# Performance work log

Measured on AMD Instinct MI355X. Metric: run time of the kernel, lower is better.

The kernel has to match this reference:

```python
import jax, jax.numpy as jnp
import numpy as np

B, N, D_MODEL = 2, 1536, 512
MIN_WL, MAX_WL, BASE = 3.7, 20.0, 20.0
COORD_SCALE = 8.0  # Angstrom-ish spread so pair distances span the wavelength band
EPS = 1e-6


def setup_inputs() -> dict:
    key = jax.random.key(0)
    k1, _ = jax.random.split(key)
    coords = jax.random.normal(k1, (B, N, 3), dtype=jnp.float32) * COORD_SCALE
    key_padding_mask = jnp.zeros((B, N), dtype=bool)  # True = padded
    K = D_MODEL // 2
    # buffer from __init__: min_wl + (max_wl-min_wl)*(logspace(0,1,K,base)-1)/(base-1)
    wavelengths = MIN_WL + (MAX_WL - MIN_WL) * (jnp.logspace(0.0, 1.0, K, base=BASE) - 1.0) / (BASE - 1.0)
    wavenumbers = (2.0 * jnp.pi / wavelengths).astype(jnp.float32)
    return {"coords": coords, "key_padding_mask": key_padding_mask, "wavenumbers": wavenumbers}


def reference(coords, key_padding_mask, wavenumbers):
    # coords: [B,N,3]; key_padding_mask: [B,N] (True = pad); wavenumbers: [K]
    b, n, _ = coords.shape
    diff = coords[:, :, None, :] - coords[:, None, :, :]          # [B,N,N,3]
    r = jnp.sqrt(jnp.sum(diff * diff, axis=-1) + 1e-12)            # [B,N,N]
    # valid sources: not padded and not the point itself (Green's fn singular at r=0)
    valid = (~key_padding_mask)[:, None, :] & (~jnp.eye(n, dtype=bool))[None]
    amp = jnp.where(valid, 1.0 / (4.0 * jnp.pi * jnp.maximum(r, EPS)), 0.0)  # [B,N,N]

    # scan over wavenumbers so we never materialize a [B,N,N,K] tensor
    def step(_, k):
        phase = k * r                                              # [B,N,N]
        re = jnp.sum(jnp.cos(phase) * amp, axis=-1)                # [B,N]
        im = jnp.sum(jnp.sin(phase) * amp, axis=-1)                # [B,N]
        return None, (re, im)

    _, (re, im) = jax.lax.scan(step, None, wavenumbers)            # each [K,B,N]
    wf = jnp.stack([re, im], axis=-1)                              # [K,B,N,2]
    wf = jnp.moveaxis(wf, 0, 2)                                    # [B,N,K,2]
    return wf.reshape(b, n, -1)                                    # [B,N,d_model]
```

## Files before the change

kernel.cpp:

```cpp
#include <hip/hip_runtime.h>
#include <math.h>


#define N_FIXED  1536
#define K_FIXED  256
#define QBINS    256
#define QG       260
#define ROWS     4
#define RSTRIDE  272
#define NTHREADS 512
#define FPSCALE  4194304.0f

typedef __attribute__((ext_vector_type(2))) float f32x2;

__global__ __launch_bounds__(256) void wf_direct_kernel(
    const float* __restrict__ coords, const unsigned char* __restrict__ mask,
    const float* __restrict__ wavenumbers, float* __restrict__ out, int N, int K)
{
    __shared__ float2 pairs[N_FIXED];
    const int row = blockIdx.x;
    const int b   = row / N;
    const int i   = row - b * N;
    const int t   = threadIdx.x;
    const float* crow = coords + (size_t)b * N * 3;
    const float xi = crow[i*3+0], yi = crow[i*3+1], zi = crow[i*3+2];
    const unsigned char* mrow = mask + (size_t)b * N;
    for (int j = t; j < N; j += blockDim.x) {
        float dx = crow[j*3+0]-xi, dy = crow[j*3+1]-yi, dz = crow[j*3+2]-zi;
        float d2 = fmaf(dx,dx, fmaf(dy,dy, fmaf(dz,dz, 1e-12f)));
        float r  = sqrtf(d2);
        float amp = 0.07957747154594767f / fmaxf(r, 1e-6f);
        if (j == i || mrow[j]) amp = 0.0f;
        pairs[j] = make_float2(r, amp);
    }
    __syncthreads();
    const int k = t;
    const float f = wavenumbers[k] * 0.15915494309189535f;
    float re = 0.0f, im = 0.0f;
    #pragma unroll 4
    for (int j = 0; j < N; ++j) {
        float2 p = pairs[j];
        float x  = __builtin_amdgcn_fractf(p.x * f);
        float c  = __builtin_amdgcn_cosf(x);
        float s  = __builtin_amdgcn_sinf(x);
        re = fmaf(c, p.y, re);
        im = fmaf(s, p.y, im);
    }
    float2* orow = (float2*)out + (size_t)row * K;
    orow[k] = make_float2(re, im);
}

__global__ __launch_bounds__(NTHREADS) void wf_fused_kernel(
    const float* __restrict__ coords, const unsigned char* __restrict__ mask,
    const float* __restrict__ wavenumbers, float* __restrict__ out, int N)
{
    __shared__ int   hist[ROWS * RSTRIDE];
    __shared__ float red[8];
    __shared__ f32x2 merge[ROWS * K_FIXED];

    const int i0 = blockIdx.x * ROWS;
    const int b  = i0 / N;
    const int t  = threadIdx.x;

    const float* crow = coords + (size_t)b * N * 3;
    const unsigned char* mrow = mask + (size_t)b * N;

    float m = 0.0f;
    #pragma unroll
    for (int s = 0; s < N_FIXED / NTHREADS; ++s) {
        const int p = t + NTHREADS * s;
        float x = crow[3*p], y = crow[3*p+1], z = crow[3*p+2];
        m = fmaxf(m, fmaf(x,x, fmaf(y,y, z*z)));
    }
    #pragma unroll
    for (int off = 32; off >= 1; off >>= 1)
        m = fmaxf(m, __shfl_down(m, off, 64));
    if ((t & 63) == 0) red[t >> 6] = m;
    for (int a = t; a < ROWS * RSTRIDE; a += NTHREADS) hist[a] = 0;
    __syncthreads();
    float mm = red[0];
    #pragma unroll
    for (int w = 1; w < 8; ++w) mm = fmaxf(mm, red[w]);
    const float rmax = 2.0005f * sqrtf(mm) + 1e-3f;
    const float h    = rmax / (float)QBINS;
    const float inv_h = 1.0f / h;

    const int il0 = i0 - b * N;
    float cx[ROWS], cy[ROWS], cz[ROWS];
    #pragma unroll
    for (int r = 0; r < ROWS; ++r) {
        cx[r] = crow[3*(il0+r)];
        cy[r] = crow[3*(il0+r)+1];
        cz[r] = crow[3*(il0+r)+2];
    }

    #pragma unroll
    for (int s = 0; s < N_FIXED / NTHREADS; ++s) {
        const int j = t + NTHREADS * s;
        const float xj = crow[3*j], yj = crow[3*j+1], zj = crow[3*j+2];
        const bool masked = (mrow[j] != 0);
        #pragma unroll
        for (int r = 0; r < ROWS; ++r) {
            float dx = xj - cx[r];
            float dy = yj - cy[r];
            float dz = zj - cz[r];
            float d2 = fmaf(dx,dx, fmaf(dy,dy, fmaf(dz,dz, 1e-12f)));
            float rsq = __builtin_amdgcn_rsqf(d2);
            float amp = 0.07957747154594767f * rsq;
            if (j == il0 + r || masked) amp = 0.0f;

            float u  = d2 * rsq * inv_h;
            float qf = floorf(u);
            int   q0 = (int)qf;
            float tt = u - qf;
            float as6 = amp * (FPSCALE * (1.0f/6.0f));
            float as2 = amp * (FPSCALE * 0.5f);
            float tm1 = tt + 1.0f, t1 = tt - 1.0f, t2 = tt - 2.0f;
            float p  = tt  * t1;
            float qq = tm1 * t2;
            int w0 = (int)(-(p  * t2)  * as6);
            int w1 = (int)( (qq * t1)  * as2);
            int w2 = (int)(-(qq * tt)  * as2);
            int w3 = (int)( (p  * tm1) * as6);
            int* hb = &hist[r * RSTRIDE + q0];
            atomicAdd(hb + 0, w0);
            atomicAdd(hb + 1, w1);
            atomicAdd(hb + 2, w2);
            atomicAdd(hb + 3, w3);
        }
    }
    __syncthreads();

    float* hf = (float*)hist;
    const float invS = 1.0f / FPSCALE;
    for (int a = t; a < ROWS * RSTRIDE; a += NTHREADS)
        hf[a] = (float)hist[a] * invS;
    __syncthreads();

    const int team = t >> 8;
    const int c    = t & 255;
    const int gbeg = team ? 33 : 0;
    const int gend = team ? 65 : 33;
    const int qs   = gbeg * 4;

    const float xrev = wavenumbers[c] * 0.15915494309189535f * h;
    const float k2s  = 2.0f * __builtin_amdgcn_cosf(__builtin_amdgcn_fractf(xrev));
    const f32x2 k2   = {k2s, k2s};
    const float aarg = __builtin_amdgcn_fractf((float)(qs - 1) * xrev);
    const float barg = __builtin_amdgcn_fractf((float)qs * xrev);
    f32x2 wa = {__builtin_amdgcn_cosf(aarg), __builtin_amdgcn_sinf(aarg)};
    f32x2 wb = {__builtin_amdgcn_cosf(barg), __builtin_amdgcn_sinf(barg)};

    f32x2 acc[ROWS];
    #pragma unroll
    for (int r = 0; r < ROWS; ++r) acc[r] = (f32x2){0.0f, 0.0f};

    #pragma unroll 2
    for (int g = gbeg; g < gend; ++g) {
        const int q0 = g * 4;
        const float4 h0 = *(const float4*)&hf[0 * RSTRIDE + q0];
        const float4 h1 = *(const float4*)&hf[1 * RSTRIDE + q0];
        const float4 h2 = *(const float4*)&hf[2 * RSTRIDE + q0];
        const float4 h3 = *(const float4*)&hf[3 * RSTRIDE + q0];
        const float r0[4] = {h0.x, h0.y, h0.z, h0.w};
        const float r1[4] = {h1.x, h1.y, h1.z, h1.w};
        const float r2[4] = {h2.x, h2.y, h2.z, h2.w};
        const float r3[4] = {h3.x, h3.y, h3.z, h3.w};
        #pragma unroll
        for (int d = 0; d < 4; ++d) {
            acc[0] = __builtin_elementwise_fma((f32x2){r0[d], r0[d]}, wa, acc[0]);
            acc[1] = __builtin_elementwise_fma((f32x2){r1[d], r1[d]}, wa, acc[1]);
            acc[2] = __builtin_elementwise_fma((f32x2){r2[d], r2[d]}, wa, acc[2]);
            acc[3] = __builtin_elementwise_fma((f32x2){r3[d], r3[d]}, wa, acc[3]);
            const f32x2 wn = __builtin_elementwise_fma(k2, wb, -wa);
            wa = wb; wb = wn;
        }
    }

    if (team == 1) {
        #pragma unroll
        for (int r = 0; r < ROWS; ++r)
            merge[r * K_FIXED + c] = acc[r];
    }
    __syncthreads();
    if (team == 0) {
        #pragma unroll
        for (int r = 0; r < ROWS; ++r) {
            const f32x2 p = merge[r * K_FIXED + c];
            const f32x2 v = acc[r] + p;
            ((float2*)out)[(size_t)(i0 + r) * K_FIXED + c] =
                make_float2(v.x, v.y);
        }
    }
}

extern "C" void kernel_launch(void* const* d_in, const int* in_sizes, int n_in,
                              void* d_out, int out_size, void* d_ws, size_t ws_size,
                              hipStream_t stream) {
    const float* coords          = (const float*)d_in[0];
    const unsigned char* mask    = (const unsigned char*)d_in[1];
    const float* wavenumbers     = (const float*)d_in[2];
    float* out                   = (float*)d_out;

    const int K  = in_sizes[2];
    const int BN = in_sizes[0] / 3;
    const int N  = N_FIXED;

    if (K != K_FIXED || BN % N != 0 || (N % ROWS) != 0 ||
        (N % NTHREADS) != 0) {
        wf_direct_kernel<<<BN, K, 0, stream>>>(coords, mask, wavenumbers, out, N, K);
        return;
    }

    wf_fused_kernel<<<BN / ROWS, NTHREADS, 0, stream>>>(coords, mask,
                                                        wavenumbers, out, N);
}
```

Before: 74.21 us.

## Halve block size and split bin range across waves with four columns per thread

```diff
diff --git a/kernel.cpp b/kernel.cpp
--- a/kernel.cpp
+++ b/kernel.cpp
@@ -8,7 +8,9 @@
 #define QG       260
 #define ROWS     4
 #define RSTRIDE  272
-#define NTHREADS 512
+#define NTHREADS 256
+#define NWAVES   (NTHREADS / 64)
+#define CPT      4
 #define FPSCALE  4194304.0f
 
 typedef __attribute__((ext_vector_type(2))) float f32x2;
@@ -55,8 +57,8 @@
     const float* __restrict__ wavenumbers, float* __restrict__ out, int N)
 {
     __shared__ int   hist[ROWS * RSTRIDE];
-    __shared__ float red[8];
-    __shared__ f32x2 merge[ROWS * K_FIXED];
+    __shared__ float red[NWAVES];
+    __shared__ f32x2 msum[ROWS * K_FIXED];
 
     const int i0 = blockIdx.x * ROWS;
     const int b  = i0 / N;
@@ -77,10 +79,14 @@
         m = fmaxf(m, __shfl_down(m, off, 64));
     if ((t & 63) == 0) red[t >> 6] = m;
     for (int a = t; a < ROWS * RSTRIDE; a += NTHREADS) hist[a] = 0;
+    {
+        float* mz = (float*)msum;
+        for (int a = t; a < ROWS * K_FIXED * 2; a += NTHREADS) mz[a] = 0.0f;
+    }
     __syncthreads();
     float mm = red[0];
     #pragma unroll
-    for (int w = 1; w < 8; ++w) mm = fmaxf(mm, red[w]);
+    for (int w = 1; w < NWAVES; ++w) mm = fmaxf(mm, red[w]);
     const float rmax = 2.0005f * sqrtf(mm) + 1e-3f;
     const float h    = rmax / (float)QBINS;
     const float inv_h = 1.0f / h;
@@ -137,23 +143,29 @@
         hf[a] = (float)hist[a] * invS;
     __syncthreads();
 
-    const int team = t >> 8;
-    const int c    = t & 255;
-    const int gbeg = team ? 33 : 0;
-    const int gend = team ? 65 : 33;
+    const int wv   = t >> 6;
+    const int c0   = t & 63;
+    const int gbeg = (wv == 0) ? 0 : (16 * wv + 1);
+    const int gend = 16 * wv + 17;
     const int qs   = gbeg * 4;
 
-    const float xrev = wavenumbers[c] * 0.15915494309189535f * h;
-    const float k2s  = 2.0f * __builtin_amdgcn_cosf(__builtin_amdgcn_fractf(xrev));
-    const f32x2 k2   = {k2s, k2s};
-    const float aarg = __builtin_amdgcn_fractf((float)(qs - 1) * xrev);
-    const float barg = __builtin_amdgcn_fractf((float)qs * xrev);
-    f32x2 wa = {__builtin_amdgcn_cosf(aarg), __builtin_amdgcn_sinf(aarg)};
-    f32x2 wb = {__builtin_amdgcn_cosf(barg), __builtin_amdgcn_sinf(barg)};
-
-    f32x2 acc[ROWS];
-    #pragma unroll
-    for (int r = 0; r < ROWS; ++r) acc[r] = (f32x2){0.0f, 0.0f};
+    f32x2 k2[CPT], wa[CPT], wb[CPT];
+    #pragma unroll
+    for (int cc = 0; cc < CPT; ++cc) {
+        const float xr  = wavenumbers[c0 + 64 * cc] * 0.15915494309189535f * h;
+        const float k2s = 2.0f * __builtin_amdgcn_cosf(__builtin_amdgcn_fractf(xr));
+        k2[cc] = (f32x2){k2s, k2s};
+        const float aarg = __builtin_amdgcn_fractf((float)(qs - 1) * xr);
+        const float barg = __builtin_amdgcn_fractf((float)qs * xr);
+        wa[cc] = (f32x2){__builtin_amdgcn_cosf(aarg), __builtin_amdgcn_sinf(aarg)};
+        wb[cc] = (f32x2){__builtin_amdgcn_cosf(barg), __builtin_amdgcn_sinf(barg)};
+    }
+
+    f32x2 acc[CPT][ROWS];
+    #pragma unroll
+    for (int cc = 0; cc < CPT; ++cc)
+        #pragma unroll
+        for (int r = 0; r < ROWS; ++r) acc[cc][r] = (f32x2){0.0f, 0.0f};
 
     #pragma unroll 2
     for (int g = gbeg; g < gend; ++g) {
@@ -168,29 +180,38 @@
         const float r3[4] = {h3.x, h3.y, h3.z, h3.w};
         #pragma unroll
         for (int d = 0; d < 4; ++d) {
-            acc[0] = __builtin_elementwise_fma((f32x2){r0[d], r0[d]}, wa, acc[0]);
-            acc[1] = __builtin_elementwise_fma((f32x2){r1[d], r1[d]}, wa, acc[1]);
-            acc[2] = __builtin_elementwise_fma((f32x2){r2[d], r2[d]}, wa, acc[2]);
-            acc[3] = __builtin_elementwise_fma((f32x2){r3[d], r3[d]}, wa, acc[3]);
-            const f32x2 wn = __builtin_elementwise_fma(k2, wb, -wa);
-            wa = wb; wb = wn;
+            const f32x2 s0 = {r0[d], r0[d]};
+            const f32x2 s1 = {r1[d], r1[d]};
+            const f32x2 s2 = {r2[d], r2[d]};
+            const f32x2 s3 = {r3[d], r3[d]};
+            #pragma unroll
+            for (int cc = 0; cc < CPT; ++cc) {
+                acc[cc][0] = __builtin_elementwise_fma(s0, wa[cc], acc[cc][0]);
+                acc[cc][1] = __builtin_elementwise_fma(s1, wa[cc], acc[cc][1]);
+                acc[cc][2] = __builtin_elementwise_fma(s2, wa[cc], acc[cc][2]);
+                acc[cc][3] = __builtin_elementwise_fma(s3, wa[cc], acc[cc][3]);
+                const f32x2 wn = __builtin_elementwise_fma(k2[cc], wb[cc], -wa[cc]);
+                wa[cc] = wb[cc]; wb[cc] = wn;
+            }
         }
     }
 
-    if (team == 1) {
-        #pragma unroll
-        for (int r = 0; r < ROWS; ++r)
-            merge[r * K_FIXED + c] = acc[r];
-    }
-    __syncthreads();
-    if (team == 0) {
+    float* msumf = (float*)msum;
+    #pragma unroll
+    for (int cc = 0; cc < CPT; ++cc) {
+        const int col = c0 + 64 * cc;
         #pragma unroll
         for (int r = 0; r < ROWS; ++r) {
-            const f32x2 p = merge[r * K_FIXED + c];
-            const f32x2 v = acc[r] + p;
-            ((float2*)out)[(size_t)(i0 + r) * K_FIXED + c] =
-                make_float2(v.x, v.y);
+            atomicAdd(&msumf[(r * K_FIXED + col) * 2 + 0], acc[cc][r].x);
+            atomicAdd(&msumf[(r * K_FIXED + col) * 2 + 1], acc[cc][r].y);
         }
+    }
+    __syncthreads();
+
+    for (int idx = t; idx < ROWS * K_FIXED; idx += NTHREADS) {
+        const f32x2 v = msum[idx];
+        ((float2*)out)[(size_t)(i0 + (idx >> 8)) * K_FIXED + (idx & 255)] =
+            make_float2(v.x, v.y);
     }
 }
 
```

Result: slower. 105.5 us (+42.1%).

## Split histogram into two row pairs and overlap deposit with contraction

Applied to the files above, without the earlier changes.

```diff
diff --git a/kernel.cpp b/kernel.cpp
--- a/kernel.cpp
+++ b/kernel.cpp
@@ -54,7 +54,8 @@
     const float* __restrict__ coords, const unsigned char* __restrict__ mask,
     const float* __restrict__ wavenumbers, float* __restrict__ out, int N)
 {
-    __shared__ int   hist[ROWS * RSTRIDE];
+    __shared__ int   histA[2 * RSTRIDE];
+    __shared__ int   histB[2 * RSTRIDE];
     __shared__ float red[8];
     __shared__ f32x2 merge[ROWS * K_FIXED];
 
@@ -76,7 +77,7 @@
     for (int off = 32; off >= 1; off >>= 1)
         m = fmaxf(m, __shfl_down(m, off, 64));
     if ((t & 63) == 0) red[t >> 6] = m;
-    for (int a = t; a < ROWS * RSTRIDE; a += NTHREADS) hist[a] = 0;
+    for (int a = t; a < 2 * RSTRIDE; a += NTHREADS) { histA[a] = 0; histB[a] = 0; }
     __syncthreads();
     float mm = red[0];
     #pragma unroll
@@ -85,113 +86,130 @@
     const float h    = rmax / (float)QBINS;
     const float inv_h = 1.0f / h;
 
+    const int qh   = t >> 8;
+    const int c    = t & 255;
+    const int gbeg = qh ? 33 : 0;
+    const int gend = qh ? 65 : 33;
+    const int qs   = gbeg * 4;
+
+    const float xr  = wavenumbers[c] * 0.15915494309189535f * h;
+    const float k2s = 2.0f * __builtin_amdgcn_cosf(__builtin_amdgcn_fractf(xr));
+    const f32x2 k2  = {k2s, k2s};
+    const float aarg = __builtin_amdgcn_fractf((float)(qs - 1) * xr);
+    const float barg = __builtin_amdgcn_fractf((float)qs * xr);
+    const f32x2 wa_s = {__builtin_amdgcn_cosf(aarg), __builtin_amdgcn_sinf(aarg)};
+    const f32x2 wb_s = {__builtin_amdgcn_cosf(barg), __builtin_amdgcn_sinf(barg)};
+
     const int il0 = i0 - b * N;
-    float cx[ROWS], cy[ROWS], cz[ROWS];
-    #pragma unroll
-    for (int r = 0; r < ROWS; ++r) {
-        cx[r] = crow[3*(il0+r)];
-        cy[r] = crow[3*(il0+r)+1];
-        cz[r] = crow[3*(il0+r)+2];
-    }
-
-    #pragma unroll
-    for (int s = 0; s < N_FIXED / NTHREADS; ++s) {
-        const int j = t + NTHREADS * s;
-        const float xj = crow[3*j], yj = crow[3*j+1], zj = crow[3*j+2];
-        const bool masked = (mrow[j] != 0);
-        #pragma unroll
-        for (int r = 0; r < ROWS; ++r) {
-            float dx = xj - cx[r];
-            float dy = yj - cy[r];
-            float dz = zj - cz[r];
-            float d2 = fmaf(dx,dx, fmaf(dy,dy, fmaf(dz,dz, 1e-12f)));
-            float rsq = __builtin_amdgcn_rsqf(d2);
-            float amp = 0.07957747154594767f * rsq;
-            if (j == il0 + r || masked) amp = 0.0f;
-
-            float u  = d2 * rsq * inv_h;
-            float qf = floorf(u);
-            int   q0 = (int)qf;
-            float tt = u - qf;
-            float as6 = amp * (FPSCALE * (1.0f/6.0f));
-            float as2 = amp * (FPSCALE * 0.5f);
-            float tm1 = tt + 1.0f, t1 = tt - 1.0f, t2 = tt - 2.0f;
-            float p  = tt  * t1;
-            float qq = tm1 * t2;
-            int w0 = (int)(-(p  * t2)  * as6);
-            int w1 = (int)( (qq * t1)  * as2);
-            int w2 = (int)(-(qq * tt)  * as2);
-            int w3 = (int)( (p  * tm1) * as6);
-            int* hb = &hist[r * RSTRIDE + q0];
-            atomicAdd(hb + 0, w0);
-            atomicAdd(hb + 1, w1);
-            atomicAdd(hb + 2, w2);
-            atomicAdd(hb + 3, w3);
-        }
-    }
-    __syncthreads();
-
-    float* hf = (float*)hist;
-    const float invS = 1.0f / FPSCALE;
-    for (int a = t; a < ROWS * RSTRIDE; a += NTHREADS)
-        hf[a] = (float)hist[a] * invS;
-    __syncthreads();
-
-    const int team = t >> 8;
-    const int c    = t & 255;
-    const int gbeg = team ? 33 : 0;
-    const int gend = team ? 65 : 33;
-    const int qs   = gbeg * 4;
-
-    const float xrev = wavenumbers[c] * 0.15915494309189535f * h;
-    const float k2s  = 2.0f * __builtin_amdgcn_cosf(__builtin_amdgcn_fractf(xrev));
-    const f32x2 k2   = {k2s, k2s};
-    const float aarg = __builtin_amdgcn_fractf((float)(qs - 1) * xrev);
-    const float barg = __builtin_amdgcn_fractf((float)qs * xrev);
-    f32x2 wa = {__builtin_amdgcn_cosf(aarg), __builtin_amdgcn_sinf(aarg)};
-    f32x2 wb = {__builtin_amdgcn_cosf(barg), __builtin_amdgcn_sinf(barg)};
-
-    f32x2 acc[ROWS];
-    #pragma unroll
-    for (int r = 0; r < ROWS; ++r) acc[r] = (f32x2){0.0f, 0.0f};
-
-    #pragma unroll 2
-    for (int g = gbeg; g < gend; ++g) {
-        const int q0 = g * 4;
-        const float4 h0 = *(const float4*)&hf[0 * RSTRIDE + q0];
-        const float4 h1 = *(const float4*)&hf[1 * RSTRIDE + q0];
-        const float4 h2 = *(const float4*)&hf[2 * RSTRIDE + q0];
-        const float4 h3 = *(const float4*)&hf[3 * RSTRIDE + q0];
-        const float r0[4] = {h0.x, h0.y, h0.z, h0.w};
-        const float r1[4] = {h1.x, h1.y, h1.z, h1.w};
-        const float r2[4] = {h2.x, h2.y, h2.z, h2.w};
-        const float r3[4] = {h3.x, h3.y, h3.z, h3.w};
-        #pragma unroll
-        for (int d = 0; d < 4; ++d) {
-            acc[0] = __builtin_elementwise_fma((f32x2){r0[d], r0[d]}, wa, acc[0]);
-            acc[1] = __builtin_elementwise_fma((f32x2){r1[d], r1[d]}, wa, acc[1]);
-            acc[2] = __builtin_elementwise_fma((f32x2){r2[d], r2[d]}, wa, acc[2]);
-            acc[3] = __builtin_elementwise_fma((f32x2){r3[d], r3[d]}, wa, acc[3]);
-            const f32x2 wn = __builtin_elementwise_fma(k2, wb, -wa);
-            wa = wb; wb = wn;
-        }
-    }
-
-    if (team == 1) {
-        #pragma unroll
-        for (int r = 0; r < ROWS; ++r)
-            merge[r * K_FIXED + c] = acc[r];
-    }
-    __syncthreads();
-    if (team == 0) {
-        #pragma unroll
-        for (int r = 0; r < ROWS; ++r) {
-            const f32x2 p = merge[r * K_FIXED + c];
-            const f32x2 v = acc[r] + p;
-            ((float2*)out)[(size_t)(i0 + r) * K_FIXED + c] =
-                make_float2(v.x, v.y);
-        }
-    }
+#define DEPOSIT_PAIR(HIST, ROW0)                                              \
+    {                                                                         \
+        const float c0x = crow[3*(il0+(ROW0))],                               \
+                    c0y = crow[3*(il0+(ROW0))+1],                             \
+                    c0z = crow[3*(il0+(ROW0))+2];                             \
+        const float c1x = crow[3*(il0+(ROW0)+1)],                             \
+                    c1y = crow[3*(il0+(ROW0)+1)+1],                           \
+                    c1z = crow[3*(il0+(ROW0)+1)+2];                           \
+        _Pragma("unroll")                                                     \
+        for (int s = 0; s < N_FIXED / NTHREADS; ++s) {                        \
+            const int j = t + NTHREADS * s;                                   \
+            const float xj = crow[3*j], yj = crow[3*j+1], zj = crow[3*j+2];   \
+            const bool masked = (mrow[j] != 0);                               \
+            _Pragma("unroll")                                                 \
+            for (int r = 0; r < 2; ++r) {                                     \
+                const float cxr = r ? c1x : c0x;                              \
+                const float cyr = r ? c1y : c0y;                              \
+                const float czr = r ? c1z : c0z;                              \
+                float dx = xj - cxr;                                          \
+                float dy = yj - cyr;                                          \
+                float dz = zj - czr;                                          \
+                float d2 = fmaf(dx,dx, fmaf(dy,dy, fmaf(dz,dz, 1e-12f)));     \
+                float rsq = __builtin_amdgcn_rsqf(d2);                        \
+                float amp = 0.07957747154594767f * rsq;                       \
+                if (j == il0 + (ROW0) + r || masked) amp = 0.0f;              \
+                float u  = d2 * rsq * inv_h;                                  \
+                float qf = floorf(u);                                         \
+                int   q0 = (int)qf;                                           \
+                float tt = u - qf;                                            \
+                float as6 = amp * (FPSCALE * (1.0f/6.0f));                    \
+                float as2 = amp * (FPSCALE * 0.5f);                           \
+                float tm1 = tt + 1.0f, t1 = tt - 1.0f, t2 = tt - 2.0f;        \
+                float p  = tt  * t1;                                          \
+                float qq = tm1 * t2;                                          \
+                int w0 = (int)(-(p  * t2)  * as6);                            \
+                int w1 = (int)( (qq * t1)  * as2);                            \
+                int w2 = (int)(-(qq * tt)  * as2);                            \
+                int w3 = (int)( (p  * tm1) * as6);                            \
+                int* hb = &(HIST)[r * RSTRIDE + q0];                          \
+                atomicAdd(hb + 0, w0);                                        \
+                atomicAdd(hb + 1, w1);                                        \
+                atomicAdd(hb + 2, w2);                                        \
+                atomicAdd(hb + 3, w3);                                        \
+            }                                                                 \
+        }                                                                     \
+    }
+
+#define CONTRACT_PAIR(HIST, ACC0, ACC1, WA, WB)                               \
+    {                                                                         \
+        _Pragma("unroll 2")                                                   \
+        for (int g = gbeg; g < gend; ++g) {                                   \
+            const int q0 = g * 4;                                             \
+            const int4 ia = *(const int4*)&(HIST)[0 * RSTRIDE + q0];          \
+            const int4 ib = *(const int4*)&(HIST)[1 * RSTRIDE + q0];          \
+            const float ra[4] = {(float)ia.x, (float)ia.y,                    \
+                                 (float)ia.z, (float)ia.w};                   \
+            const float rb[4] = {(float)ib.x, (float)ib.y,                    \
+                                 (float)ib.z, (float)ib.w};                   \
+            _Pragma("unroll")                                                 \
+            for (int d = 0; d < 4; ++d) {                                     \
+                const f32x2 sa = {ra[d], ra[d]};                              \
+                const f32x2 sb = {rb[d], rb[d]};                              \
+                ACC0 = __builtin_elementwise_fma(sa, WA, ACC0);               \
+                ACC1 = __builtin_elementwise_fma(sb, WA, ACC1);               \
+                const f32x2 wn = __builtin_elementwise_fma(k2, WB, -WA);      \
+                WA = WB; WB = wn;                                             \
+            }                                                                 \
+        }                                                                     \
+    }
+
+    f32x2 acc0 = {0.f,0.f}, acc1 = {0.f,0.f};
+    f32x2 acc2 = {0.f,0.f}, acc3 = {0.f,0.f};
+
+    DEPOSIT_PAIR(histA, 0)
+    __syncthreads();
+
+    DEPOSIT_PAIR(histB, 2)
+    {
+        f32x2 wa = wa_s, wb = wb_s;
+        CONTRACT_PAIR(histA, acc0, acc1, wa, wb)
+    }
+    __syncthreads();
+
+    {
+        f32x2 wa = wa_s, wb = wb_s;
+        CONTRACT_PAIR(histB, acc2, acc3, wa, wb)
+    }
+
+    if (qh == 1) {
+        merge[0 * K_FIXED + c] = acc0;
+        merge[1 * K_FIXED + c] = acc1;
+        merge[2 * K_FIXED + c] = acc2;
+        merge[3 * K_FIXED + c] = acc3;
+    }
+    __syncthreads();
+    if (qh == 0) {
+        const float invS = 1.0f / FPSCALE;
+        const f32x2 sS = {invS, invS};
+        const f32x2 v0 = (acc0 + merge[0 * K_FIXED + c]) * sS;
+        const f32x2 v1 = (acc1 + merge[1 * K_FIXED + c]) * sS;
+        const f32x2 v2 = (acc2 + merge[2 * K_FIXED + c]) * sS;
+        const f32x2 v3 = (acc3 + merge[3 * K_FIXED + c]) * sS;
+        ((float2*)out)[(size_t)(i0 + 0) * K_FIXED + c] = make_float2(v0.x, v0.y);
+        ((float2*)out)[(size_t)(i0 + 1) * K_FIXED + c] = make_float2(v1.x, v1.y);
+        ((float2*)out)[(size_t)(i0 + 2) * K_FIXED + c] = make_float2(v2.x, v2.y);
+        ((float2*)out)[(size_t)(i0 + 3) * K_FIXED + c] = make_float2(v3.x, v3.y);
+    }
+#undef DEPOSIT_PAIR
+#undef CONTRACT_PAIR
 }
 
 extern "C" void kernel_launch(void* const* d_in, const int* in_sizes, int n_in,
```

After: 80.82 us. 1.09x slower.
